# Optimization experiments

Hardware: AMD Instinct MI355X
Metric: run time of the kernel (lower is better)

The kernel has to match this reference:

```python
import jax, jax.numpy as jnp
import numpy as np

B, N_IN, N_OUT, C = 4, 512, 1024, 64
INIT_LENGTH_SCALE = 0.1


def setup_inputs() -> dict:
    key = jax.random.key(0)
    k1, k2, k3, k4, k5 = jax.random.split(key, 5)
    x = jax.random.uniform(k1, (B, N_IN, 1), dtype=jnp.float32)
    y = jax.random.normal(k2, (B, N_IN, C), dtype=jnp.float32)
    t = jax.random.uniform(k3, (B, N_OUT, 1), dtype=jnp.float32)
    # learnable params: per-channel log length-scale, pointwise linear C -> 1
    sigma = jnp.full((C,), np.log(INIT_LENGTH_SCALE), dtype=jnp.float32)
    w = jax.random.normal(k4, (C, 1), dtype=jnp.float32) / np.sqrt(C)
    b = jnp.zeros((1,), dtype=jnp.float32)
    return {"x": x, "y": y, "t": t, "sigma": sigma, "w": w, "b": b}


def reference(x, y, t, sigma, w, b):
    # pairwise squared distances: (B, n_in, n_out)
    dists = (x - jnp.swapaxes(t, 1, 2)) ** 2
    scales = jnp.exp(sigma)  # (C,)
    # RBF weights, broadcast over channels: (B, n_in, n_out, C)
    wt = jnp.exp(-0.5 * dists[..., None] / scales**2)
    # weighted sum over input points: (B, n_out, C)
    y_out = jnp.einsum("bnc,bnmc->bmc", y, wt)
    # pointwise linear C -> 1: (B, n_out, 1)
    return y_out @ w + b
```

## Files before the change

### kernel.cpp

```cpp
#include <hip/hip_runtime.h>

constexpr int Bb   = 4;
constexpr int NIN  = 512;
constexpr int NOUT = 1024;
constexpr int CC   = 64;

constexpr int NSPLIT = 8;
constexpr int NCHUNK = NIN / NSPLIT;
constexpr int MPB    = 256;
constexpr int MBLK   = NOUT / MPB;

__global__ __launch_bounds__(256) void rbf_prep(
    const float* __restrict__ y, const float* __restrict__ w,
    float* __restrict__ ytil)
{
    const int lane = threadIdx.x & 63;
    const int i    = blockIdx.x * 4 + (threadIdx.x >> 6);
    float v = y[(size_t)i * CC + lane] * w[lane];
#pragma unroll
    for (int off = 32; off > 0; off >>= 1) v += __shfl_xor(v, off, 64);
    if (lane == 0) ytil[i] = v;
}

__global__ __launch_bounds__(256) void rbf_main(
    const float* __restrict__ x,     const float* __restrict__ y,
    const float* __restrict__ t,     const float* __restrict__ sigma,
    const float* __restrict__ w,     const float* __restrict__ bias,
    const float* __restrict__ ytil,  float* __restrict__ out)
{
    const int tid   = threadIdx.x;
    const int lane  = tid & 63;
    const int bi    = blockIdx.x;
    const int split = bi & (NSPLIT - 1);
    const int mb    = (bi >> 3) & (MBLK - 1);
    const int b     = bi >> 5;
    const int n0    = split * NCHUNK;

    const float s0 = sigma[0];
    const bool uni = (__ballot(sigma[lane] == s0) == ~0ull);

    if (uni) {
        const int   m  = mb * MPB + tid;
        const float s  = 0.84932180f * __expf(-s0);
        const float tm = t[b * NOUT + m] * s;
        const float* __restrict__ xb = x    + b * NIN + n0;
        const float* __restrict__ yb = ytil + b * NIN + n0;
        float acc = 0.f;
#pragma unroll 8
        for (int n = 0; n < NCHUNK; ++n) {
            const float d = xb[n] * s - tm;
            acc += __builtin_amdgcn_exp2f(-(d * d)) * yb[n];
        }
        atomicAdd(out + b * NOUT + m, acc + (split == 0 ? bias[0] : 0.f));
    } else {
        const int   wv  = tid >> 6;
        const float kc2 = -0.72134752f * __expf(-2.0f * sigma[lane]);
        const float wc  = w[lane];
        const float* __restrict__ xb = x + b * NIN + n0;
        const float* __restrict__ yb = y + ((size_t)b * NIN + n0) * CC + lane;
        for (int j = 0; j < 64; ++j) {
            const int   m  = mb * MPB + wv * 64 + j;
            const float tm = t[b * NOUT + m];
            float acc = 0.f;
            for (int n = 0; n < NCHUNK; ++n) {
                const float d = xb[n] - tm;
                acc += __builtin_amdgcn_exp2f(d * d * kc2) * yb[(size_t)n * CC];
            }
            float p = acc * wc;
#pragma unroll
            for (int off = 32; off > 0; off >>= 1) p += __shfl_xor(p, off, 64);
            if (lane == 0)
                atomicAdd(out + b * NOUT + m, p + (split == 0 ? bias[0] : 0.f));
        }
    }
}

extern "C" void kernel_launch(void* const* d_in, const int* in_sizes, int n_in,
                              void* d_out, int out_size, void* d_ws, size_t ws_size,
                              hipStream_t stream) {
    const float* x     = (const float*)d_in[0];
    const float* y     = (const float*)d_in[1];
    const float* t     = (const float*)d_in[2];
    const float* sigma = (const float*)d_in[3];
    const float* w     = (const float*)d_in[4];
    const float* bias  = (const float*)d_in[5];
    float* out  = (float*)d_out;
    float* ytil = (float*)d_ws;

    hipMemsetAsync(out, 0, (size_t)out_size * sizeof(float), stream);

    rbf_prep<<<Bb * NIN / 4, 256, 0, stream>>>(y, w, ytil);

    const int grid = Bb * MBLK * NSPLIT;
    rbf_main<<<grid, MPB, 0, stream>>>(x, y, t, sigma, w, bias, ytil, out);
}
```

Before: 68.72 us.

## Replace atomic split-N reduction with in-block shared-memory reduction and drop memset

Each block now handles 64 output points and splits the 512 inputs across its 4 waves, combining the partial sums in shared memory and writing the output directly. This removes the hipMemsetAsync launch and the global atomicAdds. The inner loop gains four independent accumulators to expose more instruction-level parallelism. The grid shrinks from 128 to 64 blocks, which lowers occupancy on a large GPU, and the non-uniform path now loops over all 512 inputs per block.

```diff
diff --git a/kernel.cpp b/kernel.cpp
--- a/kernel.cpp
+++ b/kernel.cpp
@@ -5,10 +5,9 @@
 constexpr int NOUT = 1024;
 constexpr int CC   = 64;
 
-constexpr int NSPLIT = 8;
-constexpr int NCHUNK = NIN / NSPLIT;
-constexpr int MPB    = 256;
-constexpr int MBLK   = NOUT / MPB;
+constexpr int MTILE = 64;
+constexpr int NGRP  = 4;
+constexpr int NPER  = NIN / NGRP;
 
 __global__ __launch_bounds__(256) void rbf_prep(
     const float* __restrict__ y, const float* __restrict__ w,
@@ -28,49 +27,58 @@
     const float* __restrict__ w,     const float* __restrict__ bias,
     const float* __restrict__ ytil,  float* __restrict__ out)
 {
-    const int tid   = threadIdx.x;
-    const int lane  = tid & 63;
-    const int bi    = blockIdx.x;
-    const int split = bi & (NSPLIT - 1);
-    const int mb    = (bi >> 3) & (MBLK - 1);
-    const int b     = bi >> 5;
-    const int n0    = split * NCHUNK;
+    __shared__ float part[NGRP * MTILE];
+    const int tid  = threadIdx.x;
+    const int lane = tid & 63;
+    const int g    = tid >> 6;
+    const int mt   = blockIdx.x & 15;
+    const int b    = blockIdx.x >> 4;
+    const int m    = mt * MTILE + lane;
 
-    const float s0 = sigma[0];
-    const bool uni = (__ballot(sigma[lane] == s0) == ~0ull);
+    const float s0  = sigma[0];
+    const bool  uni = (__ballot(sigma[lane] == s0) == ~0ull);
 
     if (uni) {
-        const int   m  = mb * MPB + tid;
         const float s  = 0.84932180f * __expf(-s0);
         const float tm = t[b * NOUT + m] * s;
-        const float* __restrict__ xb = x    + b * NIN + n0;
-        const float* __restrict__ yb = ytil + b * NIN + n0;
-        float acc = 0.f;
+        const float* __restrict__ xb = x    + b * NIN + g * NPER;
+        const float* __restrict__ yb = ytil + b * NIN + g * NPER;
+        float a0 = 0.f, a1 = 0.f, a2 = 0.f, a3 = 0.f;
 #pragma unroll 8
-        for (int n = 0; n < NCHUNK; ++n) {
-            const float d = xb[n] * s - tm;
-            acc += __builtin_amdgcn_exp2f(-(d * d)) * yb[n];
+        for (int n = 0; n < NPER; n += 4) {
+            const float d0 = xb[n + 0] * s - tm;
+            const float d1 = xb[n + 1] * s - tm;
+            const float d2 = xb[n + 2] * s - tm;
+            const float d3 = xb[n + 3] * s - tm;
+            a0 += __builtin_amdgcn_exp2f(-(d0 * d0)) * yb[n + 0];
+            a1 += __builtin_amdgcn_exp2f(-(d1 * d1)) * yb[n + 1];
+            a2 += __builtin_amdgcn_exp2f(-(d2 * d2)) * yb[n + 2];
+            a3 += __builtin_amdgcn_exp2f(-(d3 * d3)) * yb[n + 3];
         }
-        atomicAdd(out + b * NOUT + m, acc + (split == 0 ? bias[0] : 0.f));
+        part[tid] = (a0 + a1) + (a2 + a3);
+        __syncthreads();
+        if (g == 0) {
+            const float r = (part[lane] + part[64 + lane]) +
+                            (part[128 + lane] + part[192 + lane]) + bias[0];
+            out[b * NOUT + m] = r;
+        }
     } else {
-        const int   wv  = tid >> 6;
         const float kc2 = -0.72134752f * __expf(-2.0f * sigma[lane]);
         const float wc  = w[lane];
-        const float* __restrict__ xb = x + b * NIN + n0;
-        const float* __restrict__ yb = y + ((size_t)b * NIN + n0) * CC + lane;
-        for (int j = 0; j < 64; ++j) {
-            const int   m  = mb * MPB + wv * 64 + j;
-            const float tm = t[b * NOUT + m];
+        const float* __restrict__ xb = x + b * NIN;
+        const float* __restrict__ yb = y + (size_t)b * NIN * CC + lane;
+        for (int j = 0; j < 16; ++j) {
+            const int   mm = mt * MTILE + g * 16 + j;
+            const float tm = t[b * NOUT + mm];
             float acc = 0.f;
-            for (int n = 0; n < NCHUNK; ++n) {
+            for (int n = 0; n < NIN; ++n) {
                 const float d = xb[n] - tm;
                 acc += __builtin_amdgcn_exp2f(d * d * kc2) * yb[(size_t)n * CC];
             }
             float p = acc * wc;
 #pragma unroll
             for (int off = 32; off > 0; off >>= 1) p += __shfl_xor(p, off, 64);
-            if (lane == 0)
-                atomicAdd(out + b * NOUT + m, p + (split == 0 ? bias[0] : 0.f));
+            if (lane == 0) out[b * NOUT + mm] = p + bias[0];
         }
     }
 }
@@ -87,10 +95,6 @@
     float* out  = (float*)d_out;
     float* ytil = (float*)d_ws;
 
-    hipMemsetAsync(out, 0, (size_t)out_size * sizeof(float), stream);
-
     rbf_prep<<<Bb * NIN / 4, 256, 0, stream>>>(y, w, ytil);
-
-    const int grid = Bb * MBLK * NSPLIT;
-    rbf_main<<<grid, MPB, 0, stream>>>(x, y, t, sigma, w, bias, ytil, out);
+    rbf_main<<<Bb * (NOUT / MTILE), 256, 0, stream>>>(x, y, t, sigma, w, bias, ytil, out);
 }
```

Result: no change. 67.41 us (-1.9%).
